# Kernel tuning notes

Measured on AMD Instinct MI355X. Metric: run time of the kernel, lower is better.

Reference implementation:

```python
import jax, jax.numpy as jnp
import numpy as np
from jax import lax

B, C_G, H, W = 2, 64, 240, 1216
NUM, K, IDX_REF = 8, 9, 4  # prop_kernel=3
PROP_TIME = 6


def conv3x3(x, w, b):
    y = lax.conv_general_dilated(x, w, (1, 1), ((1, 1), (1, 1)),
                                 dimension_numbers=('NCHW', 'OIHW', 'NCHW'))
    return y + b[None, :, None, None]


def bilinear_sample(img, y, x):
    """img: (B,H,W); y,x: (B,K,H,W) absolute coords; zero padding outside."""
    Hh, Ww = img.shape[1], img.shape[2]
    y0 = jnp.floor(y)
    x0 = jnp.floor(x)
    wy1, wx1 = y - y0, x - x0
    gather = jax.vmap(lambda im, a, b: im[a, b])
    out = jnp.zeros_like(y)
    for i, (yy, wy) in enumerate(((y0, 1.0 - wy1), (y0 + 1.0, wy1))):
        for j, (xx, wx) in enumerate(((x0, 1.0 - wx1), (x0 + 1.0, wx1))):
            valid = (yy >= 0) & (yy <= Hh - 1) & (xx >= 0) & (xx <= Ww - 1)
            yi = jnp.clip(yy, 0, Hh - 1).astype(jnp.int32)
            xi = jnp.clip(xx, 0, Ww - 1).astype(jnp.int32)
            v = gather(img, yi, xi)
            out = out + wy * wx * jnp.where(valid, v, 0.0)
    return out


def setup_inputs() -> dict:
    key = jax.random.key(0)
    ks = jax.random.split(key, 6)
    return {
        'initial_disp': jax.random.uniform(ks[0], (B, 1, H, W), jnp.float32) * 50.0,
        'occlus_mask': jax.random.uniform(ks[1], (B, 1, H, W), jnp.float32),
        'confidence': jax.random.uniform(ks[2], (B, 1, H, W), jnp.float32),
        'guidance_feature': jax.random.normal(ks[3], (B, C_G, H, W), jnp.float32),
        'conv_w': 0.05 * jax.random.normal(ks[4], (3 * NUM, C_G, 3, 3), jnp.float32),
        'conv_b': jnp.zeros((3 * NUM,), jnp.float32),
        'aff_scale_const': jnp.full((1,), 0.5 * NUM, jnp.float32),  # TGASS: gamma*num
    }


def nlspn_forward(initial_disp, occlus_mask, confidence, guidance_feature,
                  conv_w, conv_b, aff_scale_const):
    Bb, _, Hh, Ww = guidance_feature.shape
    oa = conv3x3(guidance_feature, conv_w, conv_b)          # (B, 3*num, H, W)
    o1, o2, aff = oa[:, :NUM], oa[:, NUM:2 * NUM], oa[:, 2 * NUM:]
    off = jnp.concatenate([o1, o2], axis=1).reshape(Bb, NUM, 2, Hh, Ww)
    zero = jnp.zeros((Bb, 1, 2, Hh, Ww), off.dtype)
    off = jnp.concatenate([off[:, :IDX_REF], zero, off[:, IDX_REF:]], axis=1)  # (B,9,2,H,W)

    # TGASS affinity
    aff = jnp.tanh(aff) / (aff_scale_const[0] + 1e-8)       # (B,8,H,W)

    gy = jnp.arange(Hh, dtype=jnp.float32)[None, None, :, None]
    gx = jnp.arange(Ww, dtype=jnp.float32)[None, None, None, :]

    # confidence sampling: 1x1 deform conv (w_conf=1, bias=0), detached offsets
    off_sg = lax.stop_gradient(off)
    nb = jnp.array([0, 1, 2, 3, 5, 6, 7, 8])
    conf_s = bilinear_sample(confidence[:, 0],
                             gy + off_sg[:, nb, 0], gx + off_sg[:, nb, 1])  # (B,8,H,W)
    aff = aff * conf_s

    s = jnp.sum(jnp.abs(aff), axis=1, keepdims=True) + 1e-5
    s = jnp.where(s < 1.0, 1.0, s)
    aff = aff / s
    aff_ref = 1.0 - jnp.sum(aff, axis=1, keepdims=True)
    aff_full = jnp.concatenate([aff[:, :IDX_REF], aff_ref, aff[:, IDX_REF:]], axis=1)  # (B,9,H,W)

    # 3x3 deform conv grid (stride 1, pad 1, dil 1), weight=ones, bias=0
    kh = (jnp.arange(K) // 3 - 1).astype(jnp.float32).reshape(1, K, 1, 1)
    kw = (jnp.arange(K) % 3 - 1).astype(jnp.float32).reshape(1, K, 1, 1)
    sy = gy + kh + off[:, :, 0]
    sx = gx + kw + off[:, :, 1]

    disp = initial_disp
    list_disp = []
    for _ in range(PROP_TIME):
        samp = bilinear_sample(disp[:, 0], sy, sx)           # (B,9,H,W)
        disp = jnp.sum(aff_full * samp, axis=1, keepdims=True)
        disp = jnp.maximum(disp, 0.0)
        disp = (1.0 - occlus_mask) * disp + occlus_mask * initial_disp
        list_disp.append(disp)
    disp = jnp.maximum(disp, 0.0)

    offset_flat = off.reshape(Bb, 2 * K, Hh, Ww)
    return disp, jnp.stack(list_disp), offset_flat, aff_full, aff_scale_const


def reference(initial_disp, occlus_mask, confidence, guidance_feature,
              conv_w, conv_b, aff_scale_const):
    return nlspn_forward(initial_disp, occlus_mask, confidence, guidance_feature,
                         conv_w, conv_b, aff_scale_const)
```

## Files before the change

### kernel.cpp

```cpp
#include <hip/hip_runtime.h>
#include <hip/hip_bf16.h>
#include <math.h>
#include <string.h>

typedef __attribute__((ext_vector_type(8))) short bf16x8;
typedef __attribute__((ext_vector_type(4))) float f32x4;

constexpr int Bc = 2, CGc = 64, Hc = 240, Wc = 1216;
constexpr int IDXR = 4, PROP = 6;
constexpr long HW  = (long)Hc * Wc;
constexpr long BHW = (long)Bc * HW;

constexpr long OUT0 = 0;
constexpr long OUT1 = BHW;
constexpr long OUT2 = BHW * 7;
constexpr long OUT3 = OUT2 + (long)Bc * 18 * HW;
constexpr long OUT4 = OUT3 + (long)Bc * 9 * HW;

constexpr int HP = Hc + 2, WPAD = Wc + 2;
constexpr long APXB   = (long)HP * WPAD;
constexpr long A_TOT  = (long)Bc * APXB * 128;
constexpr long WOFF   = A_TOT;
constexpr long WS_NEED = WOFF + (long)9 * 32 * 128;

constexpr int PR = 4, PC = 64, HLO = 6;
constexpr int TR = PR + 2 * HLO;
constexpr int TC = PC + 2 * HLO + 1;

__device__ __forceinline__ unsigned short f2bf(float f) {
  __hip_bfloat16 h = __float2bfloat16(f);
  return __builtin_bit_cast(unsigned short, h);
}

__device__ __forceinline__ void row2(const float* __restrict__ img, int yy, int x0,
                                     float& a, float& b) {
  if (yy >= 0 && yy < Hc) {
    if (x0 >= 0 && x0 < Wc - 1) {
      float2 v;
      __builtin_memcpy(&v, img + (long)yy * Wc + x0, 8);
      a = v.x; b = v.y;
    } else {
      a = (x0 >= 0 && x0 < Wc)         ? img[(long)yy * Wc + x0]     : 0.f;
      b = (x0 + 1 >= 0 && x0 + 1 < Wc) ? img[(long)yy * Wc + x0 + 1] : 0.f;
    }
  } else { a = 0.f; b = 0.f; }
}

__device__ __forceinline__ float bilin(const float* __restrict__ img, float y, float x) {
  float y0f = floorf(y), x0f = floorf(x);
  int y0 = (int)y0f, x0 = (int)x0f;
  float wy = y - y0f, wx = x - x0f;
  float v00, v01, v10, v11;
  row2(img, y0,     x0, v00, v01);
  row2(img, y0 + 1, x0, v10, v11);
  float top = v00 + wx * (v01 - v00);
  float bot = v10 + wx * (v11 - v10);
  return top + wy * (bot - top);
}

__device__ __forceinline__ float bilin_tile(
    const float (*tile)[TC], const float* __restrict__ db,
    int y0, int x0, float sy, float sx) {
  float yf = floorf(sy), xf = floorf(sx);
  int iy = (int)yf, ix = (int)xf;
  float wy = sy - yf, wx = sx - xf;
  if (iy >= y0 - HLO && iy + 1 <= y0 + PR - 1 + HLO &&
      ix >= x0 - HLO && ix + 1 <= x0 + PC - 1 + HLO) {
    int ly = iy - (y0 - HLO), lx = ix - (x0 - HLO);
    float v00 = tile[ly][lx],     v01 = tile[ly][lx + 1];
    float v10 = tile[ly + 1][lx], v11 = tile[ly + 1][lx + 1];
    float top = v00 + wx * (v01 - v00);
    float bot = v10 + wx * (v11 - v10);
    return top + wy * (bot - top);
  }
  return bilin(db, sy, sx);
}

__device__ __forceinline__ void stage_tile(
    float (*tile)[TC], const float* __restrict__ db, int y0, int x0, int tid) {
  for (int i = tid; i < TR * TC; i += 256) {
    int rr = i / TC, cc = i - rr * TC;
    int gy = y0 - HLO + rr, gx = x0 - HLO + cc;
    tile[rr][cc] = (gy >= 0 && gy < Hc && gx >= 0 && gx < Wc)
                       ? db[(long)gy * Wc + gx] : 0.f;
  }
}

__global__ __launch_bounds__(256) void nhwc_kernel(
    const float* __restrict__ g, char* __restrict__ ws) {
  __shared__ __align__(16) char tileb[64 * 132];
  const int tid = threadIdx.x;
  const int x0 = blockIdx.x * 64;
  const int y  = blockIdx.y;
  const int bz = blockIdx.z;
  const float* gb = g + (long)bz * CGc * HW + (long)y * Wc + x0;
  const int px = tid & 63, wv = tid >> 6;
#pragma unroll
  for (int k = 0; k < 16; ++k) {
    int ic = k * 4 + wv;
    float v = gb[(long)ic * HW + px];
    *reinterpret_cast<unsigned short*>(tileb + px * 132 + ic * 2) = f2bf(v);
  }
  __syncthreads();
  const int opx = tid >> 2, q = tid & 3;
  unsigned int u[8];
#pragma unroll
  for (int j = 0; j < 8; ++j)
    u[j] = *reinterpret_cast<unsigned int*>(tileb + opx * 132 + q * 32 + j * 4);
  char* dst = ws + ((long)(bz * HP + y + 1) * WPAD + x0 + 1 + opx) * 128 + q * 32;
  reinterpret_cast<uint4*>(dst)[0] = make_uint4(u[0], u[1], u[2], u[3]);
  reinterpret_cast<uint4*>(dst)[1] = make_uint4(u[4], u[5], u[6], u[7]);
}

__global__ __launch_bounds__(256) void border_kernel(char* __restrict__ ws) {
  constexpr int NB = 2 * WPAD + 2 * (HP - 2);
  long i = (long)blockIdx.x * 256 + threadIdx.x;
  if (i >= (long)Bc * NB) return;
  int bz = (int)(i / NB);
  int r  = (int)(i - (long)bz * NB);
  int py, px;
  if (r < WPAD)            { py = 0;      px = r; }
  else if (r < 2 * WPAD)   { py = HP - 1; px = r - WPAD; }
  else { int qq = r - 2 * WPAD; py = 1 + (qq >> 1); px = (qq & 1) ? (WPAD - 1) : 0; }
  char* p = ws + ((long)(bz * HP + py) * WPAD + px) * 128;
  uint4 z = make_uint4(0, 0, 0, 0);
#pragma unroll
  for (int j = 0; j < 8; ++j) reinterpret_cast<uint4*>(p)[j] = z;
}

__global__ __launch_bounds__(256) void wconv_kernel(
    const float* __restrict__ w, char* __restrict__ ws) {
  char* wd = ws + WOFF;
  int idx = blockIdx.x * 256 + threadIdx.x;
  if (idx < 24 * 64 * 9) {
    int oc = idx / 576, r = idx - oc * 576;
    int ic = r / 9, tap = r - ic * 9;
    *reinterpret_cast<unsigned short*>(wd + tap * 4096 + oc * 128 + ic * 2) = f2bf(w[idx]);
  } else if (idx < 32 * 64 * 9) {
    int i2 = idx - 24 * 64 * 9;
    int oc = 24 + i2 / 576, r = i2 % 576;
    int ic = r / 9, tap = r % 9;
    *reinterpret_cast<unsigned short*>(wd + tap * 4096 + oc * 128 + ic * 2) = 0;
  }
}

constexpr int CTILE_BYTES = 6 * 66 * 128;
constexpr int CUNITS = CTILE_BYTES / 16;
constexpr int EXCH_BYTES = 4 * 64 * 25 * 4;
constexpr int DT_OFF = EXCH_BYTES;
constexpr int CT_OFF = DT_OFF + TR * TC * 4;

__global__ __launch_bounds__(256) void conv_fused_kernel(
    const char* __restrict__ ws, const float* __restrict__ bias,
    const float* __restrict__ conf, const float* __restrict__ scale_p,
    const float* __restrict__ occm, const float* __restrict__ initd,
    float* __restrict__ out) {
  __shared__ __align__(16) char smemA[CTILE_BYTES];
  const int tid  = threadIdx.x;
  const int lane = tid & 63, wv = tid >> 6;
  const int lrow = lane & 15, lgrp = lane >> 4;
  const int x0 = blockIdx.x * 64;
  const int y0 = blockIdx.y * 4;
  const int bz = blockIdx.z;

  const char* Abase = ws + ((long)(bz * HP + y0) * WPAD + x0) * 128;
#pragma unroll
  for (int it = 0; it < 13; ++it) {
    int u = it * 256 + tid;
    if (u < CUNITS) {
      int pxl = u >> 3, j = u & 7;
      int r = pxl / 66, col = pxl - r * 66;
      uint4 v = *reinterpret_cast<const uint4*>(
          Abase + ((long)r * WPAD + col) * 128 + j * 16);
      int ldsb = pxl * 128 + ((j ^ (col & 7)) << 4);
      *reinterpret_cast<uint4*>(smemA + ldsb) = v;
    }
  }
  __syncthreads();

  const char* Wb = ws + WOFF + (long)lrow * 128 + lgrp * 16;

  f32x4 acc[4][2];
#pragma unroll
  for (int h = 0; h < 4; ++h)
#pragma unroll
    for (int nt = 0; nt < 2; ++nt) acc[h][nt] = (f32x4){0.f, 0.f, 0.f, 0.f};

#pragma unroll
  for (int tap = 0; tap < 9; ++tap) {
    const int dy = tap / 3, dx = tap - dy * 3;
    const char* Wt = Wb + tap * 4096;
#pragma unroll
    for (int ks = 0; ks < 2; ++ks) {
      bf16x8 wf0 = *reinterpret_cast<const bf16x8*>(Wt + ks * 64);
      bf16x8 wf1 = *reinterpret_cast<const bf16x8*>(Wt + 2048 + ks * 64);
#pragma unroll
      for (int h = 0; h < 4; ++h) {
        const int colc = lrow + dx + h * 16;
        int abyte = ((wv + dy) * 66 + colc) * 128 +
                    ((((ks << 2) + lgrp) ^ (colc & 7)) << 4);
        bf16x8 af = *reinterpret_cast<const bf16x8*>(smemA + abyte);
        acc[h][0] = __builtin_amdgcn_mfma_f32_16x16x32_bf16(af, wf0, acc[h][0], 0, 0, 0);
        acc[h][1] = __builtin_amdgcn_mfma_f32_16x16x32_bf16(af, wf1, acc[h][1], 0, 0, 0);
      }
    }
  }
  __syncthreads();

  float* exch = reinterpret_cast<float*>(smemA);
  {
    const int y = y0 + wv;
#pragma unroll
    for (int h = 0; h < 4; ++h) {
      const int xx = x0 + h * 16 + lgrp * 4;
      const int lpx = h * 16 + lgrp * 4;
#pragma unroll
      for (int nt = 0; nt < 2; ++nt) {
        int oc = nt * 16 + lrow;
        if (oc >= 24) continue;
        float bv = bias[oc];
        f32x4 v = acc[h][nt];
#pragma unroll
        for (int j = 0; j < 4; ++j)
          exch[(wv * 64 + lpx + j) * 25 + oc] = v[j] + bv;
        if (oc < 16) {
          int n = oc >> 1, cd = oc & 1;
          int mm = (n < IDXR) ? n : n + 1;
          long dst = OUT2 + (long)(bz * 18 + 2 * mm + cd) * HW;
          float4 st = make_float4(v[0] + bv, v[1] + bv, v[2] + bv, v[3] + bv);
          *reinterpret_cast<float4*>(&out[dst + (long)y * Wc + xx]) = st;
        }
      }
    }
  }
  __syncthreads();

  float (*dtile)[TC] = reinterpret_cast<float (*)[TC]>(smemA + DT_OFF);
  float (*ctile)[TC] = reinterpret_cast<float (*)[TC]>(smemA + CT_OFF);
  const float* db    = initd + (long)bz * HW;
  const float* confb = conf  + (long)bz * HW;
  stage_tile(dtile, db,    y0, x0, tid);
  stage_tile(ctile, confb, y0, x0, tid);
  __syncthreads();

  const int row = tid >> 6, px = tid & 63;
  const int y = y0 + row, x = x0 + px;
  long rem = (long)y * Wc + x;
  long p = (long)bz * HW + rem;

  float ch[24];
#pragma unroll
  for (int j = 0; j < 24; ++j) ch[j] = exch[(row * 64 + px) * 25 + j];

  const float inv_scale = 1.f / (scale_p[0] + 1e-8f);
  float* off  = out + OUT2 + (long)bz * 18 * HW + rem;
  float* affp = out + OUT3 + (long)bz * 9  * HW + rem;

  float affr[9], oyr[9], oxr[9];
  float asum = 0.f;
#pragma unroll
  for (int m = 0; m < 8; m++) {
    int n = (m < IDXR) ? m : m + 1;
    float oy  = ch[2 * m];
    float ox  = ch[2 * m + 1];
    float raw = ch[16 + m];
    float avv = tanhf(raw) * inv_scale;
    float cs  = bilin_tile(ctile, confb, y0, x0, (float)y + oy, (float)x + ox);
    affr[n] = avv * cs;
    oyr[n] = oy; oxr[n] = ox;
    asum += fabsf(affr[n]);
  }
  float s = fmaxf(asum + 1e-5f, 1.0f);
  float inv_s = 1.f / s;
  float total = 0.f;
#pragma unroll
  for (int m = 0; m < 8; m++) {
    int n = (m < IDXR) ? m : m + 1;
    affr[n] *= inv_s; total += affr[n];
  }
  affr[IDXR] = 1.f - total;
  oyr[IDXR] = 0.f; oxr[IDXR] = 0.f;
#pragma unroll
  for (int n = 0; n < 9; n++) affp[(long)n * HW] = affr[n];
  off[(long)(2 * IDXR) * HW]     = 0.f;
  off[(long)(2 * IDXR + 1) * HW] = 0.f;
  if (p == 0) out[OUT4] = scale_p[0];

  float occv  = occm[p];
  float initv = db[rem];
  float acc0 = 0.f;
#pragma unroll
  for (int k = 0; k < 9; k++) {
    float sy = (float)(y + k / 3 - 1) + oyr[k];
    float sx = (float)(x + k % 3 - 1) + oxr[k];
    acc0 = fmaf(affr[k], bilin_tile(dtile, db, y0, x0, sy, sx), acc0);
  }
  acc0 = fmaxf(acc0, 0.f);
  out[OUT1 + p] = (1.f - occv) * acc0 + occv * initv;
}

__global__ __launch_bounds__(256) void prop_tile_kernel(
    const float* __restrict__ dispPrev,
    const float* __restrict__ occ, const float* __restrict__ initd,
    float* __restrict__ out, int t) {
  __shared__ float tile[TR][TC];
  const int tid = threadIdx.x;
  const int x0 = blockIdx.x * PC;
  const int y0 = blockIdx.y * PR;
  const int b  = blockIdx.z;
  const float* db = dispPrev + (long)b * HW;
  stage_tile(tile, db, y0, x0, tid);
  __syncthreads();

  const int y = y0 + (tid >> 6);
  const int x = x0 + (tid & 63);
  long rem = (long)y * Wc + x;
  long p = (long)b * HW + rem;

  const float* off  = out + OUT2 + (long)b * 18 * HW + rem;
  const float* affp = out + OUT3 + (long)b * 9  * HW + rem;

  float acc = 0.f;
#pragma unroll
  for (int k = 0; k < 9; k++) {
    float oy = off[(long)(2 * k) * HW];
    float ox = off[(long)(2 * k + 1) * HW];
    float av = affp[(long)k * HW];
    float sy = (float)(y + k / 3 - 1) + oy;
    float sx = (float)(x + k % 3 - 1) + ox;
    acc = fmaf(av, bilin_tile(tile, db, y0, x0, sy, sx), acc);
  }
  acc = fmaxf(acc, 0.f);
  float o = occ[p];
  float res = (1.f - o) * acc + o * initd[p];
  out[OUT1 + (long)t * BHW + p] = res;
  if (t == PROP - 1) out[OUT0 + p] = res;
}

constexpr int TY = 8, TX = 32;
constexpr int AR = TY + 2, AC = TX + 2;
constexpr int A_BYTES = AR * AC * CGc * 2;
constexpr int W_BYTES = 9 * 32 * 32 * 2;

__global__ __launch_bounds__(256) void conv_mfma_kernel(
    const float* __restrict__ g, const float* __restrict__ wsrc,
    const float* __restrict__ bias, float* __restrict__ out) {
  __shared__ __align__(16) char smemA[A_BYTES];
  __shared__ __align__(16) char smemW[W_BYTES];
  const int tid = threadIdx.x;
  const int x0 = blockIdx.x * TX;
  const int y0 = blockIdx.y * TY;
  const int bz = blockIdx.z;
  const float* gb = g + (long)bz * CGc * HW;
  for (int w = tid; w < AR * AC * 32; w += 256) {
    int c  = w % AC;
    int t2 = w / AC;
    int icp = t2 & 31;
    int r   = t2 >> 5;
    int y = y0 + r - 1, x = x0 + c - 1;
    float v0 = 0.f, v1 = 0.f;
    if (y >= 0 && y < Hc && x >= 0 && x < Wc) {
      const float* p = gb + (long)(2 * icp) * HW + (long)y * Wc + x;
      v0 = p[0]; v1 = p[HW];
    }
    unsigned int pk = (unsigned int)f2bf(v0) | ((unsigned int)f2bf(v1) << 16);
    int byte = (r * AC + c) * 128 + icp * 4;
    byte ^= (c & 7) << 4;
    *reinterpret_cast<unsigned int*>(smemA + byte) = pk;
  }
  auto stageW = [&](int hs) {
    for (int idx = tid; idx < 24 * 32 * 9; idx += 256) {
      int oc  = idx / 288;
      int r1  = idx - oc * 288;
      int icl = r1 / 9;
      int tap = r1 - icl * 9;
      float f = wsrc[idx + 288 * (oc + hs)];
      int byte = (tap * 32 + oc) * 64 + icl * 2;
      byte ^= (oc & 7) << 4;
      *reinterpret_cast<unsigned short*>(smemW + byte) = f2bf(f);
    }
  };
  stageW(0);
  __syncthreads();
  const int wid  = tid >> 6;
  const int lane = tid & 63;
  const int lrow = lane & 15;
  const int lgrp = lane >> 4;
  f32x4 acc[4][2];
#pragma unroll
  for (int m = 0; m < 4; m++)
#pragma unroll
    for (int nt = 0; nt < 2; nt++) acc[m][nt] = (f32x4){0.f, 0.f, 0.f, 0.f};
  for (int ks = 0; ks < 2; ++ks) {
    if (ks) { __syncthreads(); stageW(1); __syncthreads(); }
#pragma unroll
    for (int tap = 0; tap < 9; ++tap) {
      const int dy = tap / 3, dx = tap - dy * 3;
      int bb = (tap * 32 + lrow) * 64 + lgrp * 16;
      int bbyte0 = bb ^ ((lrow & 7) << 4);
      int bbyte1 = (bb + 16 * 64) ^ ((lrow & 7) << 4);
      bf16x8 bf0 = *reinterpret_cast<const bf16x8*>(smemW + bbyte0);
      bf16x8 bf1 = *reinterpret_cast<const bf16x8*>(smemW + bbyte1);
#pragma unroll
      for (int dr = 0; dr < 2; ++dr) {
        const int rin = 2 * wid + dr + dy;
#pragma unroll
        for (int h = 0; h < 2; ++h) {
          const int cin = h * 16 + lrow + dx;
          int abyte = ((rin * AC + cin) * 128 + ks * 64 + lgrp * 16) ^ ((cin & 7) << 4);
          bf16x8 af = *reinterpret_cast<const bf16x8*>(smemA + abyte);
          acc[dr * 2 + h][0] = __builtin_amdgcn_mfma_f32_16x16x32_bf16(af, bf0, acc[dr * 2 + h][0], 0, 0, 0);
          acc[dr * 2 + h][1] = __builtin_amdgcn_mfma_f32_16x16x32_bf16(af, bf1, acc[dr * 2 + h][1], 0, 0, 0);
        }
      }
    }
  }
#pragma unroll
  for (int dr = 0; dr < 2; ++dr) {
    const int yy = y0 + 2 * wid + dr;
#pragma unroll
    for (int h = 0; h < 2; ++h) {
      const int xx = x0 + h * 16 + lgrp * 4;
#pragma unroll
      for (int nt = 0; nt < 2; ++nt) {
        int oc = nt * 16 + lrow;
        if (oc >= 24) continue;
        float bv = bias[oc];
        long dst;
        if (oc < 16) {
          int n = oc >> 1, cd = oc & 1;
          int mm = (n < IDXR) ? n : n + 1;
          dst = OUT2 + (long)(bz * 18 + 2 * mm + cd) * HW;
        } else {
          int i2 = oc - 16;
          int mm = (i2 < IDXR) ? i2 : i2 + 1;
          dst = OUT3 + (long)(bz * 9 + mm) * HW;
        }
        f32x4 v = acc[dr * 2 + h][nt];
        float4 st = make_float4(v[0] + bv, v[1] + bv, v[2] + bv, v[3] + bv);
        *reinterpret_cast<float4*>(&out[dst + (long)yy * Wc + xx]) = st;
      }
    }
  }
}

__global__ __launch_bounds__(256) void prep_kernel(
    const float* __restrict__ conf, const float* __restrict__ scale_p,
    float* __restrict__ out) {
  long p = (long)blockIdx.x * 256 + threadIdx.x;
  if (p >= BHW) return;
  int b = (int)(p / HW);
  long rem = p - (long)b * HW;
  int y = (int)(rem / Wc);
  int x = (int)(rem - (long)y * Wc);
  const float inv_scale = 1.f / (scale_p[0] + 1e-8f);
  const float* confb = conf + (long)b * HW;
  float* off  = out + OUT2 + (long)b * 18 * HW + rem;
  float* affp = out + OUT3 + (long)b * 9  * HW + rem;
  float a[8];
  float asum = 0.f;
#pragma unroll
  for (int m = 0; m < 8; m++) {
    int n = (m < IDXR) ? m : m + 1;
    float oy  = off[(long)(2 * n) * HW];
    float ox  = off[(long)(2 * n + 1) * HW];
    float raw = affp[(long)n * HW];
    float av  = tanhf(raw) * inv_scale;
    float cs  = bilin(confb, (float)y + oy, (float)x + ox);
    a[m] = av * cs;
    asum += fabsf(a[m]);
  }
  float s = fmaxf(asum + 1e-5f, 1.0f);
  float inv_s = 1.f / s;
  float total = 0.f;
#pragma unroll
  for (int m = 0; m < 8; m++) { a[m] *= inv_s; total += a[m]; }
  float aref = 1.f - total;
#pragma unroll
  for (int m = 0; m < 8; m++) {
    int n = (m < IDXR) ? m : m + 1;
    affp[(long)n * HW] = a[m];
  }
  affp[(long)IDXR * HW] = aref;
  off[(long)(2 * IDXR) * HW]     = 0.f;
  off[(long)(2 * IDXR + 1) * HW] = 0.f;
  if (p == 0) out[OUT4] = scale_p[0];
}

__global__ __launch_bounds__(256) void prop_kernel(
    const float* __restrict__ dispPrev,
    const float* __restrict__ occ, const float* __restrict__ initd,
    float* __restrict__ out, int t) {
  long p = (long)blockIdx.x * 256 + threadIdx.x;
  if (p >= BHW) return;
  int b = (int)(p / HW);
  long rem = p - (long)b * HW;
  int y = (int)(rem / Wc);
  int x = (int)(rem - (long)y * Wc);
  const float* off  = out + OUT2 + (long)b * 18 * HW + rem;
  const float* affp = out + OUT3 + (long)b * 9  * HW + rem;
  const float* db   = dispPrev + (long)b * HW;
  float acc = 0.f;
#pragma unroll
  for (int k = 0; k < 9; k++) {
    float oy = off[(long)(2 * k) * HW];
    float ox = off[(long)(2 * k + 1) * HW];
    float av = affp[(long)k * HW];
    float sy = (float)(y + k / 3 - 1) + oy;
    float sx = (float)(x + k % 3 - 1) + ox;
    acc = fmaf(av, bilin(db, sy, sx), acc);
  }
  acc = fmaxf(acc, 0.f);
  float o = occ[p];
  float res = (1.f - o) * acc + o * initd[p];
  out[OUT1 + (long)t * BHW + p] = res;
  if (t == PROP - 1) out[OUT0 + p] = res;
}

extern "C" void kernel_launch(void* const* d_in, const int* in_sizes, int n_in,
                              void* d_out, int out_size, void* d_ws, size_t ws_size,
                              hipStream_t stream) {
  const float* initd = (const float*)d_in[0];
  const float* occ   = (const float*)d_in[1];
  const float* conf  = (const float*)d_in[2];
  const float* guid  = (const float*)d_in[3];
  const float* cw    = (const float*)d_in[4];
  const float* cb    = (const float*)d_in[5];
  const float* csc   = (const float*)d_in[6];
  float* out = (float*)d_out;
  int nblk = (int)((BHW + 255) / 256);

  if (ws_size >= (size_t)WS_NEED) {
    char* ws = (char*)d_ws;
    nhwc_kernel<<<dim3(Wc / 64, Hc, Bc), 256, 0, stream>>>(guid, ws);
    border_kernel<<<(Bc * (2 * WPAD + 2 * (HP - 2)) + 255) / 256, 256, 0, stream>>>(ws);
    wconv_kernel<<<72, 256, 0, stream>>>(cw, ws);

    dim3 pgrid(Wc / PC, Hc / PR, Bc);
    conv_fused_kernel<<<pgrid, 256, 0, stream>>>(ws, cb, conf, csc, occ, initd, out);
    for (int t = 1; t < PROP; t++) {
      const float* dp = out + OUT1 + (long)(t - 1) * BHW;
      prop_tile_kernel<<<pgrid, 256, 0, stream>>>(dp, occ, initd, out, t);
    }
  } else {
    conv_mfma_kernel<<<dim3(Wc / TX, Hc / TY, Bc), 256, 0, stream>>>(guid, cw, cb, out);
    prep_kernel<<<nblk, 256, 0, stream>>>(conf, csc, out);
    for (int t = 0; t < PROP; t++) {
      const float* dp = (t == 0) ? initd : (out + OUT1 + (long)(t - 1) * BHW);
      prop_kernel<<<nblk, 256, 0, stream>>>(dp, occ, initd, out, t);
    }
  }
}
```

Before: 223.3 us.

## Pack per-pixel fp16 offsets and affinities into an interleaved table for propagation

The first propagation step now writes a per-pixel packed table holding the 9 affinities and 18 offsets as fp16, plus occlusion and initial disparity as fp32, as four uint4 planes in the workspace. Later steps read 64 bytes per pixel as vector loads instead of 29 scattered fp32 plane reads. The aim is to cut memory traffic and load-instruction count in the repeated propagation kernels. The cost is fp16 rounding of the offsets and affinities in steps 2 through 5, which may shift the sampling positions slightly, and the workspace region for the NHWC conv input gets overwritten. The exchange stride also changes from 25 to 26.

```diff
diff --git a/kernel.cpp b/kernel.cpp
--- a/kernel.cpp
+++ b/kernel.cpp
@@ -30,6 +30,13 @@
 __device__ __forceinline__ unsigned short f2bf(float f) {
   __hip_bfloat16 h = __float2bfloat16(f);
   return __builtin_bit_cast(unsigned short, h);
+}
+__device__ __forceinline__ unsigned short f2h(float f) {
+  _Float16 h = (_Float16)f;
+  return __builtin_bit_cast(unsigned short, h);
+}
+__device__ __forceinline__ float h2f(unsigned short u) {
+  return (float)__builtin_bit_cast(_Float16, u);
 }
 
 __device__ __forceinline__ void row2(const float* __restrict__ img, int yy, int x0,
@@ -146,7 +153,8 @@
 
 constexpr int CTILE_BYTES = 6 * 66 * 128;
 constexpr int CUNITS = CTILE_BYTES / 16;
-constexpr int EXCH_BYTES = 4 * 64 * 25 * 4;
+constexpr int EXST = 26;
+constexpr int EXCH_BYTES = 4 * 64 * EXST * 4;
 constexpr int DT_OFF = EXCH_BYTES;
 constexpr int CT_OFF = DT_OFF + TR * TC * 4;
 
@@ -222,7 +230,7 @@
         f32x4 v = acc[h][nt];
 #pragma unroll
         for (int j = 0; j < 4; ++j)
-          exch[(wv * 64 + lpx + j) * 25 + oc] = v[j] + bv;
+          exch[(wv * 64 + lpx + j) * EXST + oc] = v[j] + bv;
         if (oc < 16) {
           int n = oc >> 1, cd = oc & 1;
           int mm = (n < IDXR) ? n : n + 1;
@@ -250,7 +258,7 @@
 
   float ch[24];
 #pragma unroll
-  for (int j = 0; j < 24; ++j) ch[j] = exch[(row * 64 + px) * 25 + j];
+  for (int j = 0; j < 24; ++j) ch[j] = exch[(row * 64 + px) * EXST + j];
 
   const float inv_scale = 1.f / (scale_p[0] + 1e-8f);
   float* off  = out + OUT2 + (long)bz * 18 * HW + rem;
@@ -299,9 +307,67 @@
   out[OUT1 + p] = (1.f - occv) * acc0 + occv * initv;
 }
 
-__global__ __launch_bounds__(256) void prop_tile_kernel(
+__global__ __launch_bounds__(256) void prop_tab1_kernel(
     const float* __restrict__ dispPrev,
     const float* __restrict__ occ, const float* __restrict__ initd,
+    float* __restrict__ out, uint4* __restrict__ tab4) {
+  __shared__ float tile[TR][TC];
+  const int tid = threadIdx.x;
+  const int x0 = blockIdx.x * PC;
+  const int y0 = blockIdx.y * PR;
+  const int b  = blockIdx.z;
+  const float* db = dispPrev + (long)b * HW;
+  stage_tile(tile, db, y0, x0, tid);
+  __syncthreads();
+
+  const int y = y0 + (tid >> 6);
+  const int x = x0 + (tid & 63);
+  long rem = (long)y * Wc + x;
+  long p = (long)b * HW + rem;
+
+  const float* off  = out + OUT2 + (long)b * 18 * HW + rem;
+  const float* affp = out + OUT3 + (long)b * 9  * HW + rem;
+
+  float affv[9], oyv[9], oxv[9];
+#pragma unroll
+  for (int k = 0; k < 9; k++) {
+    oyv[k]  = off[(long)(2 * k) * HW];
+    oxv[k]  = off[(long)(2 * k + 1) * HW];
+    affv[k] = affp[(long)k * HW];
+  }
+  float occv  = occ[p];
+  float initv = initd[p];
+
+  float acc = 0.f;
+#pragma unroll
+  for (int k = 0; k < 9; k++) {
+    float sy = (float)(y + k / 3 - 1) + oyv[k];
+    float sx = (float)(x + k % 3 - 1) + oxv[k];
+    acc = fmaf(affv[k], bilin_tile(tile, db, y0, x0, sy, sx), acc);
+  }
+  acc = fmaxf(acc, 0.f);
+  float res = (1.f - occv) * acc + occv * initv;
+  out[OUT1 + (long)1 * BHW + p] = res;
+
+  unsigned short hs[28];
+#pragma unroll
+  for (int k = 0; k < 9; k++) {
+    hs[k] = f2h(affv[k]); hs[9 + k] = f2h(oyv[k]); hs[18 + k] = f2h(oxv[k]);
+  }
+  hs[27] = 0;
+  unsigned u[16];
+#pragma unroll
+  for (int i = 0; i < 14; i++)
+    u[i] = (unsigned)hs[2 * i] | ((unsigned)hs[2 * i + 1] << 16);
+  u[14] = __builtin_bit_cast(unsigned, occv);
+  u[15] = __builtin_bit_cast(unsigned, initv);
+#pragma unroll
+  for (int g = 0; g < 4; g++)
+    tab4[(long)g * BHW + p] = make_uint4(u[4 * g], u[4 * g + 1], u[4 * g + 2], u[4 * g + 3]);
+}
+
+__global__ __launch_bounds__(256) void prop_tabN_kernel(
+    const float* __restrict__ dispPrev, const uint4* __restrict__ tab4,
     float* __restrict__ out, int t) {
   __shared__ float tile[TR][TC];
   const int tid = threadIdx.x;
@@ -317,22 +383,30 @@
   long rem = (long)y * Wc + x;
   long p = (long)b * HW + rem;
 
-  const float* off  = out + OUT2 + (long)b * 18 * HW + rem;
-  const float* affp = out + OUT3 + (long)b * 9  * HW + rem;
+  unsigned u[16];
+#pragma unroll
+  for (int g = 0; g < 4; g++) {
+    uint4 q = tab4[(long)g * BHW + p];
+    u[4 * g] = q.x; u[4 * g + 1] = q.y; u[4 * g + 2] = q.z; u[4 * g + 3] = q.w;
+  }
+  float fl[27];
+#pragma unroll
+  for (int i = 0; i < 27; i++) {
+    unsigned w0 = u[i >> 1];
+    fl[i] = h2f((unsigned short)((i & 1) ? (w0 >> 16) : (w0 & 0xffff)));
+  }
+  float occv  = __builtin_bit_cast(float, u[14]);
+  float initv = __builtin_bit_cast(float, u[15]);
 
   float acc = 0.f;
 #pragma unroll
   for (int k = 0; k < 9; k++) {
-    float oy = off[(long)(2 * k) * HW];
-    float ox = off[(long)(2 * k + 1) * HW];
-    float av = affp[(long)k * HW];
-    float sy = (float)(y + k / 3 - 1) + oy;
-    float sx = (float)(x + k % 3 - 1) + ox;
-    acc = fmaf(av, bilin_tile(tile, db, y0, x0, sy, sx), acc);
+    float sy = (float)(y + k / 3 - 1) + fl[9 + k];
+    float sx = (float)(x + k % 3 - 1) + fl[18 + k];
+    acc = fmaf(fl[k], bilin_tile(tile, db, y0, x0, sy, sx), acc);
   }
   acc = fmaxf(acc, 0.f);
-  float o = occ[p];
-  float res = (1.f - o) * acc + o * initd[p];
+  float res = (1.f - occv) * acc + occv * initv;
   out[OUT1 + (long)t * BHW + p] = res;
   if (t == PROP - 1) out[OUT0 + p] = res;
 }
@@ -538,9 +612,12 @@
 
     dim3 pgrid(Wc / PC, Hc / PR, Bc);
     conv_fused_kernel<<<pgrid, 256, 0, stream>>>(ws, cb, conf, csc, occ, initd, out);
-    for (int t = 1; t < PROP; t++) {
+
+    uint4* tab4 = (uint4*)ws;
+    prop_tab1_kernel<<<pgrid, 256, 0, stream>>>(out + OUT1, occ, initd, out, tab4);
+    for (int t = 2; t < PROP; t++) {
       const float* dp = out + OUT1 + (long)(t - 1) * BHW;
-      prop_tile_kernel<<<pgrid, 256, 0, stream>>>(dp, occ, initd, out, t);
+      prop_tabN_kernel<<<pgrid, 256, 0, stream>>>(dp, tab4, out, t);
     }
   } else {
     conv_mfma_kernel<<<dim3(Wc / TX, Hc / TY, Bc), 256, 0, stream>>>(guid, cw, cb, out);
```

Result: faster. 201.3 us (-9.8%).
